# Kernel tuning notes

Measured on AMD Instinct MI355X. Metric: run time of the kernel, lower is better.

## Reference

```python
import jax, jax.numpy as jnp
import numpy as np

NUM_HEADS = 16
HEAD_DIM = 80  # head_dim_ori; NPU pads 80->128 with zeros (math-neutral)


def _rotate_half(x):
    x1, x2 = jnp.split(x, 2, axis=-1)
    return jnp.concatenate([-x2, x1], axis=-1)


def setup_inputs() -> dict:
    key = jax.random.key(0)
    ks = jax.random.split(key, 7)
    S, E = 4096, 1280
    inv = jnp.asarray(1.0 / np.sqrt(E), jnp.float32)
    # rotary tables: proper cos/sin from angles for realism
    pos = jnp.arange(S, dtype=jnp.float32)[:, None]
    freqs = 1.0 / (10000.0 ** (jnp.arange(0, HEAD_DIM // 2, dtype=jnp.float32) / (HEAD_DIM // 2)))
    ang = pos * freqs[None, :]                      # [S, 40]
    ang = jnp.concatenate([ang, ang], axis=-1)      # [S, 80] rotate-half layout
    return {
        'hidden_states': jax.random.normal(ks[0], (S, E), jnp.float32),
        'cos': jnp.cos(ang),
        'sin': jnp.sin(ang),
        'w_qkv': jax.random.normal(ks[1], (3 * E, E), jnp.float32) * inv,
        'b_qkv': jax.random.normal(ks[2], (3 * E,), jnp.float32) * 0.02,
        'w_proj': jax.random.normal(ks[3], (E, E), jnp.float32) * inv,
        'b_proj': jax.random.normal(ks[4], (E,), jnp.float32) * 0.02,
    }


def reference(hidden_states, cos, sin, w_qkv, b_qkv, w_proj, b_proj):
    S, E = hidden_states.shape
    H, D = NUM_HEADS, HEAD_DIM
    # fused QKV linear (transposeB=True, hasBias=True) then split into 3
    qkv = hidden_states @ w_qkv.T + b_qkv          # [S, 3E]
    q, k, v = jnp.split(qkv, 3, axis=-1)
    q = q.reshape(S, H, D)
    k = k.reshape(S, H, D)
    v = v.reshape(S, H, D)
    # rotate-half RoPE (rotaryCoeff=2) on q and k
    c = cos[:, None, :]
    s = sin[:, None, :]
    q = q * c + _rotate_half(q) * s
    k = k * c + _rotate_half(k) * s
    # full bidirectional self-attention (PA_ENCODER), qkScale = 1/sqrt(head_dim_ori)
    scale = jnp.asarray(1.0 / np.sqrt(D), q.dtype)
    scores = jnp.einsum('shd,thd->hst', q, k) * scale   # [H, S, S]
    attn = jax.nn.softmax(scores, axis=-1)
    out = jnp.einsum('hst,thd->shd', attn, v).reshape(S, E)
    # output projection + residual add (atten_res_add)
    dense = out @ w_proj.T + b_proj
    return hidden_states + dense
```

## Files before the change

### kernel.cpp

```cpp
#include <hip/hip_runtime.h>
#include <hip/hip_bf16.h>


#define S_LEN 4096
#define E_DIM 1280
#define NH 16
#define HD 80
#define HDP 96

typedef __bf16 bf16x8 __attribute__((ext_vector_type(8)));
typedef float f32x4 __attribute__((ext_vector_type(4)));

__device__ __forceinline__ short f2bf(float x) {
    __hip_bfloat16 h = __float2bfloat16(x);
    return __builtin_bit_cast(short, h);
}
__device__ __forceinline__ float bf2f(short x) {
    return __bfloat162float(__builtin_bit_cast(__hip_bfloat16, x));
}
__device__ __forceinline__ bf16x8 ldb(const short* p) {
    return *reinterpret_cast<const bf16x8*>(p);
}
__device__ __forceinline__ unsigned cvt_pk_bf16(float a, float b) {
    unsigned r;
    asm("v_cvt_pk_bf16_f32 %0, %1, %2" : "=v"(r) : "v"(a), "v"(b));
    return r;
}
__device__ __forceinline__ void gload16(const void* g, void* l) {
    __builtin_amdgcn_global_load_lds(
        (const __attribute__((address_space(1))) unsigned int*)g,
        (__attribute__((address_space(3))) unsigned int*)l, 16, 0, 0);
}

__global__ __launch_bounds__(256) void cast3_k(const float* __restrict__ a, short* __restrict__ oa, int na4,
                                               const float* __restrict__ b, short* __restrict__ ob, int nb4,
                                               const float* __restrict__ c, short* __restrict__ oc, int nc4) {
    int j = blockIdx.x * 256 + threadIdx.x;
    const float* src;
    short* dst;
    if (j < na4) {
        src = a; dst = oa;
    } else {
        j -= na4;
        if (j < nb4) {
            src = b; dst = ob;
        } else {
            j -= nb4;
            if (j >= nc4) return;
            src = c; dst = oc;
        }
    }
    float4 v = *reinterpret_cast<const float4*>(&src[j * 4]);
    ushort4 o;
    o.x = (unsigned short)f2bf(v.x);
    o.y = (unsigned short)f2bf(v.y);
    o.z = (unsigned short)f2bf(v.z);
    o.w = (unsigned short)f2bf(v.w);
    *reinterpret_cast<ushort4*>(&dst[j * 4]) = o;
}

template <int MODE>
__global__ __launch_bounds__(256) void gemm_bt_k(
    const short* __restrict__ A, const short* __restrict__ B, const float* __restrict__ bias,
    short* __restrict__ Qraw, short* __restrict__ Kraw, short* __restrict__ Vg,
    const float* __restrict__ resid, float* __restrict__ Out) {
    const int K = E_DIM;
    __shared__ short As[2][128 * 64];
    __shared__ short Bs[2][128 * 64];
    int t = threadIdx.x;
    int lane = t & 63, w = t >> 6;
    int wr = w >> 1, wc = w & 1;
    int lr = lane & 15, lg = lane >> 4;
    int mb = blockIdx.y * 128, nb = blockIdx.x * 128;

    const short* asrc[4];
    const short* bsrc[4];
#pragma unroll
    for (int c = 0; c < 4; c++) {
        int p = c * 256 + t;
        int m = p >> 3;
        int kg = (p & 7) ^ (m & 7);
        asrc[c] = A + (size_t)(mb + m) * K + kg * 8;
        bsrc[c] = B + (size_t)(nb + m) * K + kg * 8;
    }
    int xa = lr & 7;
    int cx0 = ((0 * 4 + lg) ^ xa) * 8;
    int cx1 = ((1 * 4 + lg) ^ xa) * 8;
    int rowA[4], rowB[4];
#pragma unroll
    for (int i = 0; i < 4; i++) {
        rowA[i] = (wr * 64 + i * 16 + lr) * 64;
        rowB[i] = (wc * 64 + i * 16 + lr) * 64;
    }

    f32x4 acc[4][4];
#pragma unroll
    for (int i = 0; i < 4; i++)
#pragma unroll
        for (int j = 0; j < 4; j++) acc[i][j] = (f32x4){0.f, 0.f, 0.f, 0.f};

#define G_STAGE(buf, kb)                                             \
    {                                                                \
        _Pragma("unroll") for (int c = 0; c < 4; c++) {              \
            int ldso = c * 2048 + w * 512;                           \
            gload16(asrc[c] + (kb), &As[buf][ldso]);                 \
            gload16(bsrc[c] + (kb), &Bs[buf][ldso]);                 \
        }                                                            \
    }

    G_STAGE(0, 0);
    asm volatile("s_waitcnt vmcnt(0)" ::: "memory");
    __syncthreads();

    int buf = 0;
    for (int kb = 0; kb < K; kb += 64) {
        if (kb + 64 < K) G_STAGE(buf ^ 1, kb + 64);
        __builtin_amdgcn_s_setprio(1);
#pragma unroll
        for (int kk = 0; kk < 2; kk++) {
            int cx = kk ? cx1 : cx0;
            bf16x8 af[4], bfr[4];
#pragma unroll
            for (int i = 0; i < 4; i++) {
                af[i] = ldb(&As[buf][rowA[i] + cx]);
                bfr[i] = ldb(&Bs[buf][rowB[i] + cx]);
            }
#pragma unroll
            for (int i = 0; i < 4; i++)
#pragma unroll
                for (int j = 0; j < 4; j++)
                    acc[i][j] = __builtin_amdgcn_mfma_f32_16x16x32_bf16(af[i], bfr[j], acc[i][j], 0, 0, 0);
        }
        __builtin_amdgcn_s_setprio(0);
        __syncthreads();
        buf ^= 1;
    }
#undef G_STAGE

    if (MODE == 0) {
        int part = nb / E_DIM;
        short* dst = (part == 0) ? Qraw : (part == 1) ? Kraw : Vg;
#pragma unroll
        for (int j = 0; j < 4; j++) {
            int n = nb + wc * 64 + j * 16 + lr;
            float bv = bias[n];
            int hd = n - part * E_DIM;
            int h = hd / HD, d = hd - h * HD;
#pragma unroll
            for (int i = 0; i < 4; i++) {
#pragma unroll
                for (int r = 0; r < 4; r++) {
                    int s = mb + wr * 64 + i * 16 + lg * 4 + r;
                    dst[(h * S_LEN + s) * HD + d] = f2bf(acc[i][j][r] + bv);
                }
            }
        }
    } else {
#pragma unroll
        for (int j = 0; j < 4; j++) {
            int n = nb + wc * 64 + j * 16 + lr;
            float bv = bias[n];
#pragma unroll
            for (int i = 0; i < 4; i++) {
#pragma unroll
                for (int r = 0; r < 4; r++) {
                    int s = mb + wr * 64 + i * 16 + lg * 4 + r;
                    Out[s * E_DIM + n] = acc[i][j][r] + bv + resid[s * E_DIM + n];
                }
            }
        }
    }
}

__global__ __launch_bounds__(256) void rope_k(const short* __restrict__ Qraw,
                                              const short* __restrict__ Kraw,
                                              const float* __restrict__ cosp,
                                              const float* __restrict__ sinp,
                                              short* __restrict__ Qg, short* __restrict__ Kg) {
    int idx = blockIdx.x * 256 + threadIdx.x;
    int c = idx % 12;
    int sh = idx / 12;
    int s = sh & (S_LEN - 1);
    int base96 = sh * HDP + c * 8;
    if (c >= 10) {
        int4 z = {0, 0, 0, 0};
        *reinterpret_cast<int4*>(&Qg[base96]) = z;
        *reinterpret_cast<int4*>(&Kg[base96]) = z;
        return;
    }
    int d0 = c * 8;
    int dp = (d0 < 40) ? d0 + 40 : d0 - 40;
    float sgn = (d0 < 40) ? -1.f : 1.f;
    int base80 = sh * HD;
    float q[8], qp[8], k[8], kp[8], cs[8], sn[8];
    {
        int4 v;
        v = *reinterpret_cast<const int4*>(&Qraw[base80 + d0]);
        const short* sp = reinterpret_cast<const short*>(&v);
        for (int i = 0; i < 8; i++) q[i] = bf2f(sp[i]);
        v = *reinterpret_cast<const int4*>(&Qraw[base80 + dp]);
        for (int i = 0; i < 8; i++) qp[i] = bf2f(sp[i]);
        v = *reinterpret_cast<const int4*>(&Kraw[base80 + d0]);
        for (int i = 0; i < 8; i++) k[i] = bf2f(sp[i]);
        v = *reinterpret_cast<const int4*>(&Kraw[base80 + dp]);
        for (int i = 0; i < 8; i++) kp[i] = bf2f(sp[i]);
    }
    *reinterpret_cast<float4*>(&cs[0]) = *reinterpret_cast<const float4*>(&cosp[s * HD + d0]);
    *reinterpret_cast<float4*>(&cs[4]) = *reinterpret_cast<const float4*>(&cosp[s * HD + d0 + 4]);
    *reinterpret_cast<float4*>(&sn[0]) = *reinterpret_cast<const float4*>(&sinp[s * HD + d0]);
    *reinterpret_cast<float4*>(&sn[4]) = *reinterpret_cast<const float4*>(&sinp[s * HD + d0 + 4]);
    const float qscale = 0.16129849190f;
    short oq[8], ok[8];
#pragma unroll
    for (int i = 0; i < 8; i++) {
        oq[i] = f2bf((q[i] * cs[i] + sgn * qp[i] * sn[i]) * qscale);
        ok[i] = f2bf(k[i] * cs[i] + sgn * kp[i] * sn[i]);
    }
    *reinterpret_cast<int4*>(&Qg[base96]) = *reinterpret_cast<int4*>(oq);
    *reinterpret_cast<int4*>(&Kg[base96]) = *reinterpret_cast<int4*>(ok);
}

__global__ __launch_bounds__(256) void transpose_v_k(const short* __restrict__ Vg,
                                                     short* __restrict__ Vt) {
    __shared__ short tile[32][33];
    int h = blockIdx.z, sb = blockIdx.x * 32, db = blockIdx.y * 32;
    int t = threadIdx.x;
    for (int e = t; e < 1024; e += 256) {
        int si = e >> 5, dj = e & 31;
        int d = db + dj;
        tile[si][dj] = (d < HD) ? Vg[(h * S_LEN + sb + si) * HD + d] : (short)0;
    }
    __syncthreads();
    for (int e = t; e < 1024; e += 256) {
        int di = e >> 5, sj = e & 31;
        int d = db + di;
        if (d < HD) Vt[(h * HD + d) * S_LEN + sb + sj] = tile[sj][di];
    }
}

__global__ __launch_bounds__(512, 4) void attn_k(const short* __restrict__ Qg,
                                                 const short* __restrict__ Kg,
                                                 const short* __restrict__ Vt,
                                                 short* __restrict__ Ob) {
    __shared__ __align__(16) short smem[35072];
    short* ksb = smem;
    short* vsb = smem + 13312;
    short* psb = smem + 24832;

    int t = threadIdx.x;
    int lane = t & 63, w = t >> 6;
    int lr = lane & 15, lg = lane >> 4;
    int pairi = w >> 1, half = w & 1;
    int L = blockIdx.x;
    int h = ((L & 7) << 1) | (L >> 8);
    int qb = ((L >> 3) & 31) << 7;

    const short* kgp = Kg + (size_t)h * S_LEN * HDP;
    const short* vgp = Vt + (size_t)h * HD * S_LEN;

    bf16x8 qf[2][3];
#pragma unroll
    for (int qq = 0; qq < 2; qq++) {
        const short* qp = Qg + ((size_t)h * S_LEN + qb + pairi * 32 + qq * 16 + lr) * HDP;
#pragma unroll
        for (int kk = 0; kk < 3; kk++) qf[qq][kk] = ldb(qp + kk * 32 + lg * 8);
    }
    f32x4 o[2][5];
#pragma unroll
    for (int qq = 0; qq < 2; qq++)
#pragma unroll
        for (int nd = 0; nd < 5; nd++) o[qq][nd] = (f32x4){0.f, 0.f, 0.f, 0.f};
    f32x4 l4[2] = {(f32x4){0.f, 0.f, 0.f, 0.f}, (f32x4){0.f, 0.f, 0.f, 0.f}};

    int gk0 = t, rk0 = gk0 / 13, ok0 = gk0 % 13;
    if (ok0 == 12) ok0 = 0;
    const short* ksrc0 = kgp + rk0 * HDP + ok0 * 8;
    int gk1 = t + 512, rk1 = gk1 / 13, ok1 = gk1 % 13;
    if (ok1 == 12) ok1 = 0;
    const short* ksrc1 = kgp + rk1 * HDP + ok1 * 8;
    int gv0 = t, rv0 = gv0 / 9, ov0 = gv0 % 9;
    if (ov0 == 8) ov0 = 0;
    const short* vsrc0 = vgp + (size_t)rv0 * S_LEN + ov0 * 8;
    bool v1v = (t + 512) < 720;
    int gv1 = t + 512, rv1 = gv1 / 9, ov1 = gv1 % 9;
    if (ov1 == 8) ov1 = 0;
    const short* vsrc1 = vgp + (size_t)rv1 * S_LEN + ov1 * 8;

#define A_STAGE(buf, kb)                                                          \
    {                                                                             \
        gload16(ksrc0 + (size_t)(kb) * HDP, ksb + (buf)*6656 + w * 512);          \
        if (w < 5) gload16(ksrc1 + (size_t)(kb) * HDP, ksb + (buf)*6656 + 4096 + w * 512); \
        gload16(vsrc0 + (kb), vsb + (buf)*5760 + w * 512);                        \
        if (v1v) gload16(vsrc1 + (kb), vsb + (buf)*5760 + 4096 + w * 512);        \
    }

    A_STAGE(0, 0);
    asm volatile("s_waitcnt vmcnt(0)" ::: "memory");
    __syncthreads();

    short* ps = psb + w * 1280;
    int buf = 0;
    for (int kb = 0; kb < S_LEN; kb += 64) {
        if (kb + 64 < S_LEN) A_STAGE(buf ^ 1, kb + 64);
        const short* ks = ksb + buf * 6656;
        const short* vs = vsb + buf * 5760;

        f32x4 sc[2][2];
#pragma unroll
        for (int qq = 0; qq < 2; qq++)
#pragma unroll
            for (int n = 0; n < 2; n++) sc[qq][n] = (f32x4){0.f, 0.f, 0.f, 0.f};
        __builtin_amdgcn_s_setprio(1);
#pragma unroll
        for (int n = 0; n < 2; n++) {
#pragma unroll
            for (int kk = 0; kk < 3; kk++) {
                bf16x8 kf = ldb(&ks[(half * 32 + n * 16 + lr) * 104 + kk * 32 + lg * 8]);
                sc[0][n] = __builtin_amdgcn_mfma_f32_16x16x32_bf16(kf, qf[0][kk], sc[0][n], 0, 0, 0);
                sc[1][n] = __builtin_amdgcn_mfma_f32_16x16x32_bf16(kf, qf[1][kk], sc[1][n], 0, 0, 0);
            }
        }
        __builtin_amdgcn_s_setprio(0);

#pragma unroll
        for (int qq = 0; qq < 2; qq++) {
#pragma unroll
            for (int n = 0; n < 2; n++) {
#pragma unroll
                for (int r = 0; r < 4; r++) sc[qq][n][r] = __builtin_amdgcn_exp2f(sc[qq][n][r]);
                l4[qq] += sc[qq][n];
                uint2 pk;
                pk.x = cvt_pk_bf16(sc[qq][n][0], sc[qq][n][1]);
                pk.y = cvt_pk_bf16(sc[qq][n][2], sc[qq][n][3]);
                *reinterpret_cast<uint2*>(&ps[(qq * 16 + lr) * 40 + n * 16 + lg * 4]) = pk;
            }
        }

        bf16x8 pf0 = ldb(&ps[(0 * 16 + lr) * 40 + lg * 8]);
        bf16x8 pf1 = ldb(&ps[(1 * 16 + lr) * 40 + lg * 8]);
        __builtin_amdgcn_s_setprio(1);
#pragma unroll
        for (int nd = 0; nd < 5; nd++) {
            bf16x8 vf = ldb(&vs[(nd * 16 + lr) * 72 + half * 32 + lg * 8]);
            o[0][nd] = __builtin_amdgcn_mfma_f32_16x16x32_bf16(pf0, vf, o[0][nd], 0, 0, 0);
            o[1][nd] = __builtin_amdgcn_mfma_f32_16x16x32_bf16(pf1, vf, o[1][nd], 0, 0, 0);
        }
        __builtin_amdgcn_s_setprio(0);

        __syncthreads();
        buf ^= 1;
    }
#undef A_STAGE

    float lh[2];
#pragma unroll
    for (int qq = 0; qq < 2; qq++) {
        float l = l4[qq][0] + l4[qq][1] + l4[qq][2] + l4[qq][3];
        l += __shfl_xor(l, 16);
        l += __shfl_xor(l, 32);
        lh[qq] = l;
    }
    float* Osc = reinterpret_cast<float*>(smem);
    float* lsc = reinterpret_cast<float*>(smem) + 10240;
    if (half) {
#pragma unroll
        for (int qq = 0; qq < 2; qq++) {
#pragma unroll
            for (int nd = 0; nd < 5; nd++)
#pragma unroll
                for (int r = 0; r < 4; r++)
                    Osc[(pairi * 32 + qq * 16 + lg * 4 + r) * 80 + nd * 16 + lr] = o[qq][nd][r];
            if (lg == 0) lsc[pairi * 32 + qq * 16 + lr] = lh[qq];
        }
    }
    __syncthreads();
    if (!half) {
        float rl[2][4];
#pragma unroll
        for (int qq = 0; qq < 2; qq++) {
            float lt = lh[qq] + lsc[pairi * 32 + qq * 16 + lr];
#pragma unroll
            for (int r = 0; r < 4; r++) {
                float lf = __shfl(lt, lg * 4 + r);
                rl[qq][r] = __builtin_amdgcn_rcpf(lf);
            }
        }
#pragma unroll
        for (int qq = 0; qq < 2; qq++)
#pragma unroll
            for (int nd = 0; nd < 5; nd++)
#pragma unroll
                for (int r = 0; r < 4; r++) {
                    int s = qb + pairi * 32 + qq * 16 + lg * 4 + r;
                    float val = o[qq][nd][r] + Osc[(pairi * 32 + qq * 16 + lg * 4 + r) * 80 + nd * 16 + lr];
                    Ob[s * E_DIM + h * HD + nd * 16 + lr] = f2bf(val * rl[qq][r]);
                }
    }
}

extern "C" void kernel_launch(void* const* d_in, const int* in_sizes, int n_in,
                              void* d_out, int out_size, void* d_ws, size_t ws_size,
                              hipStream_t stream) {
    const float* hidden = (const float*)d_in[0];
    const float* cosp = (const float*)d_in[1];
    const float* sinp = (const float*)d_in[2];
    const float* wqkv = (const float*)d_in[3];
    const float* bqkv = (const float*)d_in[4];
    const float* wproj = (const float*)d_in[5];
    const float* bproj = (const float*)d_in[6];
    float* out = (float*)d_out;

    char* p = (char*)d_ws;
    short* Xb = (short*)p;      p += (size_t)S_LEN * E_DIM * 2;
    short* Wqkvb = (short*)p;   p += (size_t)3 * E_DIM * E_DIM * 2;
    short* Wprojb = (short*)p;  p += (size_t)E_DIM * E_DIM * 2;
    short* Qraw = (short*)p;    p += (size_t)NH * S_LEN * HD * 2;
    short* Kraw = (short*)p;    p += (size_t)NH * S_LEN * HD * 2;
    short* Vg = (short*)p;      p += (size_t)NH * S_LEN * HD * 2;
    short* Qg = (short*)p;      p += (size_t)NH * S_LEN * HDP * 2;
    short* Kg = (short*)p;      p += (size_t)NH * S_LEN * HDP * 2;
    short* Vt = (short*)p;      p += (size_t)NH * HD * S_LEN * 2;
    short* Ob = Xb;

    const int na4 = S_LEN * E_DIM / 4;
    const int nb4 = 3 * E_DIM * E_DIM / 4;
    const int nc4 = E_DIM * E_DIM / 4;
    cast3_k<<<(na4 + nb4 + nc4 + 255) / 256, 256, 0, stream>>>(
        hidden, Xb, na4, wqkv, Wqkvb, nb4, wproj, Wprojb, nc4);

    gemm_bt_k<0><<<dim3(3 * E_DIM / 128, S_LEN / 128), 256, 0, stream>>>(
        Xb, Wqkvb, bqkv, Qraw, Kraw, Vg, nullptr, nullptr);

    rope_k<<<NH * S_LEN * 12 / 256, 256, 0, stream>>>(Qraw, Kraw, cosp, sinp, Qg, Kg);

    transpose_v_k<<<dim3(S_LEN / 32, 3, NH), 256, 0, stream>>>(Vg, Vt);

    attn_k<<<dim3(512), 512, 0, stream>>>(Qg, Kg, Vt, Ob);

    gemm_bt_k<1><<<dim3(E_DIM / 128, S_LEN / 128), 256, 0, stream>>>(
        Ob, Wprojb, bproj, nullptr, nullptr, nullptr, hidden, out);
}
```

Before: 212.2 us.

## Add dedicated 256x256-tile QKV GEMM kernel with 8 waves and block swizzle

Replaces the templated 128x128 QKV projection GEMM with a new kernel that uses 256x256 output tiles, 512 threads (8 waves) and a hand-scheduled double-buffered LDS pipeline split into K-halves with explicit waitcnt/barriers. Blocks are remapped with a swizzle, and the grid of 240 blocks roughly matches the CU count. The larger tiles cut global and LDS traffic per FLOP, and the interleaved staging is meant to hide load latency. In exchange it uses more registers and LDS per block, and the handwritten synchronisation is fragile. The output-projection GEMM is de-templated but otherwise unchanged.

```diff
diff --git a/kernel.cpp b/kernel.cpp
--- a/kernel.cpp
+++ b/kernel.cpp
@@ -59,10 +59,171 @@
     *reinterpret_cast<ushort4*>(&dst[j * 4]) = o;
 }
 
-template <int MODE>
+__global__ __launch_bounds__(512, 2) void gemm1_256_k(
+    const short* __restrict__ A, const short* __restrict__ B, const float* __restrict__ bias,
+    short* __restrict__ Qraw, short* __restrict__ Kraw, short* __restrict__ Vg) {
+    const int K = E_DIM;
+    __shared__ short As[2][2][8192];
+    __shared__ short Bs[2][2][8192];
+    int t = threadIdx.x;
+    int lane = t & 63, w = t >> 6;
+    int wr = w >> 2, wc = w & 3;
+    int lr = lane & 15, lg = lane >> 4;
+    int bid = blockIdx.x;
+    int swz = (bid & 7) * 30 + (bid >> 3);
+    int bm = swz / 15, bn = swz % 15;
+    int mb = bm * 256, nb = bn * 256;
+
+    int lgs = (t & 3) ^ ((t >> 3) & 3);
+    const short* aS = A + (size_t)(mb + (t >> 2)) * K + lgs * 8;
+    const short* bS = B + (size_t)(nb + (t >> 2)) * K + lgs * 8;
+    const int rowStep = 128 * K;
+
+    int aoff[2][4], boff[4];
+#pragma unroll
+    for (int mq = 0; mq < 2; mq++)
+#pragma unroll
+        for (int ii = 0; ii < 4; ii++) {
+            int r = wr * 128 + mq * 64 + ii * 16 + lr;
+            aoff[mq][ii] = r * 32 + ((lg ^ ((r >> 1) & 3)) * 8);
+        }
+#pragma unroll
+    for (int n = 0; n < 4; n++) {
+        int r = wc * 64 + n * 16 + lr;
+        boff[n] = r * 32 + ((lg ^ ((r >> 1) & 3)) * 8);
+    }
+
+    f32x4 acc[8][4];
+#pragma unroll
+    for (int i = 0; i < 8; i++)
+#pragma unroll
+        for (int n = 0; n < 4; n++) acc[i][n] = (f32x4){0.f, 0.f, 0.f, 0.f};
+
+#define STG_A(d, kh, kb2)                                              \
+    {                                                                  \
+        gload16(aS + (kb2) + (kh)*32, &As[d][kh][w * 512]);            \
+        gload16(aS + rowStep + (kb2) + (kh)*32, &As[d][kh][4096 + w * 512]); \
+    }
+#define STG_B(d, kh, kb2)                                              \
+    {                                                                  \
+        gload16(bS + (kb2) + (kh)*32, &Bs[d][kh][w * 512]);            \
+        gload16(bS + rowStep + (kb2) + (kh)*32, &Bs[d][kh][4096 + w * 512]); \
+    }
+
+    STG_A(0, 0, 0);
+    STG_B(0, 0, 0);
+    STG_A(0, 1, 0);
+    STG_B(0, 1, 0);
+    asm volatile("s_waitcnt vmcnt(4)" ::: "memory");
+    __builtin_amdgcn_s_barrier();
+    asm volatile("" ::: "memory");
+
+    for (int kb = 0; kb < K; kb += 64) {
+        int d = (kb >> 6) & 1;
+        int kb2 = kb + 64;
+        bool more = kb2 < K;
+        bf16x8 af[4], bfr[4];
+
+#pragma unroll
+        for (int n = 0; n < 4; n++) bfr[n] = ldb(&Bs[d][0][boff[n]]);
+#pragma unroll
+        for (int ii = 0; ii < 4; ii++) af[ii] = ldb(&As[d][0][aoff[0][ii]]);
+        if (more) STG_A(d ^ 1, 0, kb2);
+        __builtin_amdgcn_s_barrier();
+        asm volatile("s_waitcnt lgkmcnt(0)" ::: "memory");
+        __builtin_amdgcn_sched_barrier(0);
+        __builtin_amdgcn_s_setprio(1);
+#pragma unroll
+        for (int ii = 0; ii < 4; ii++)
+#pragma unroll
+            for (int n = 0; n < 4; n++)
+                acc[ii][n] = __builtin_amdgcn_mfma_f32_16x16x32_bf16(af[ii], bfr[n], acc[ii][n], 0, 0, 0);
+        __builtin_amdgcn_s_setprio(0);
+        __builtin_amdgcn_s_barrier();
+        asm volatile("" ::: "memory");
+
+#pragma unroll
+        for (int ii = 0; ii < 4; ii++) af[ii] = ldb(&As[d][0][aoff[1][ii]]);
+        if (more) {
+            STG_B(d ^ 1, 0, kb2);
+            asm volatile("s_waitcnt vmcnt(4)" ::: "memory");
+        } else {
+            asm volatile("s_waitcnt vmcnt(0)" ::: "memory");
+        }
+        __builtin_amdgcn_s_barrier();
+        asm volatile("s_waitcnt lgkmcnt(0)" ::: "memory");
+        __builtin_amdgcn_sched_barrier(0);
+        __builtin_amdgcn_s_setprio(1);
+#pragma unroll
+        for (int ii = 0; ii < 4; ii++)
+#pragma unroll
+            for (int n = 0; n < 4; n++)
+                acc[4 + ii][n] = __builtin_amdgcn_mfma_f32_16x16x32_bf16(af[ii], bfr[n], acc[4 + ii][n], 0, 0, 0);
+        __builtin_amdgcn_s_setprio(0);
+        __builtin_amdgcn_s_barrier();
+        asm volatile("" ::: "memory");
+
+#pragma unroll
+        for (int n = 0; n < 4; n++) bfr[n] = ldb(&Bs[d][1][boff[n]]);
+#pragma unroll
+        for (int ii = 0; ii < 4; ii++) af[ii] = ldb(&As[d][1][aoff[0][ii]]);
+        if (more) STG_A(d ^ 1, 1, kb2);
+        __builtin_amdgcn_s_barrier();
+        asm volatile("s_waitcnt lgkmcnt(0)" ::: "memory");
+        __builtin_amdgcn_sched_barrier(0);
+        __builtin_amdgcn_s_setprio(1);
+#pragma unroll
+        for (int ii = 0; ii < 4; ii++)
+#pragma unroll
+            for (int n = 0; n < 4; n++)
+                acc[ii][n] = __builtin_amdgcn_mfma_f32_16x16x32_bf16(af[ii], bfr[n], acc[ii][n], 0, 0, 0);
+        __builtin_amdgcn_s_setprio(0);
+        __builtin_amdgcn_s_barrier();
+        asm volatile("" ::: "memory");
+
+#pragma unroll
+        for (int ii = 0; ii < 4; ii++) af[ii] = ldb(&As[d][1][aoff[1][ii]]);
+        if (more) {
+            STG_B(d ^ 1, 1, kb2);
+            asm volatile("s_waitcnt vmcnt(4)" ::: "memory");
+        }
+        __builtin_amdgcn_s_barrier();
+        asm volatile("s_waitcnt lgkmcnt(0)" ::: "memory");
+        __builtin_amdgcn_sched_barrier(0);
+        __builtin_amdgcn_s_setprio(1);
+#pragma unroll
+        for (int ii = 0; ii < 4; ii++)
+#pragma unroll
+            for (int n = 0; n < 4; n++)
+                acc[4 + ii][n] = __builtin_amdgcn_mfma_f32_16x16x32_bf16(af[ii], bfr[n], acc[4 + ii][n], 0, 0, 0);
+        __builtin_amdgcn_s_setprio(0);
+        __builtin_amdgcn_s_barrier();
+        asm volatile("" ::: "memory");
+    }
+#undef STG_A
+#undef STG_B
+
+    int part = nb / E_DIM;
+    short* dst = (part == 0) ? Qraw : (part == 1) ? Kraw : Vg;
+#pragma unroll
+    for (int j = 0; j < 4; j++) {
+        int n = nb + wc * 64 + j * 16 + lr;
+        float bv = bias[n];
+        int hd = n - part * E_DIM;
+        int h = hd / HD, dd = hd - h * HD;
+#pragma unroll
+        for (int i = 0; i < 8; i++) {
+#pragma unroll
+            for (int r = 0; r < 4; r++) {
+                int s = mb + wr * 128 + (i >> 2) * 64 + (i & 3) * 16 + lg * 4 + r;
+                dst[(h * S_LEN + s) * HD + dd] = f2bf(acc[i][j][r] + bv);
+            }
+        }
+    }
+}
+
 __global__ __launch_bounds__(256) void gemm_bt_k(
     const short* __restrict__ A, const short* __restrict__ B, const float* __restrict__ bias,
-    short* __restrict__ Qraw, short* __restrict__ Kraw, short* __restrict__ Vg,
     const float* __restrict__ resid, float* __restrict__ Out) {
     const int K = E_DIM;
     __shared__ short As[2][128 * 64];
@@ -137,36 +298,16 @@
     }
 #undef G_STAGE
 
-    if (MODE == 0) {
-        int part = nb / E_DIM;
-        short* dst = (part == 0) ? Qraw : (part == 1) ? Kraw : Vg;
-#pragma unroll
-        for (int j = 0; j < 4; j++) {
-            int n = nb + wc * 64 + j * 16 + lr;
-            float bv = bias[n];
-            int hd = n - part * E_DIM;
-            int h = hd / HD, d = hd - h * HD;
-#pragma unroll
-            for (int i = 0; i < 4; i++) {
-#pragma unroll
-                for (int r = 0; r < 4; r++) {
-                    int s = mb + wr * 64 + i * 16 + lg * 4 + r;
-                    dst[(h * S_LEN + s) * HD + d] = f2bf(acc[i][j][r] + bv);
-                }
-            }
-        }
-    } else {
-#pragma unroll
-        for (int j = 0; j < 4; j++) {
-            int n = nb + wc * 64 + j * 16 + lr;
-            float bv = bias[n];
-#pragma unroll
-            for (int i = 0; i < 4; i++) {
-#pragma unroll
-                for (int r = 0; r < 4; r++) {
-                    int s = mb + wr * 64 + i * 16 + lg * 4 + r;
-                    Out[s * E_DIM + n] = acc[i][j][r] + bv + resid[s * E_DIM + n];
-                }
+#pragma unroll
+    for (int j = 0; j < 4; j++) {
+        int n = nb + wc * 64 + j * 16 + lr;
+        float bv = bias[n];
+#pragma unroll
+        for (int i = 0; i < 4; i++) {
+#pragma unroll
+            for (int r = 0; r < 4; r++) {
+                int s = mb + wr * 64 + i * 16 + lg * 4 + r;
+                Out[s * E_DIM + n] = acc[i][j][r] + bv + resid[s * E_DIM + n];
             }
         }
     }
@@ -428,8 +569,7 @@
     cast3_k<<<(na4 + nb4 + nc4 + 255) / 256, 256, 0, stream>>>(
         hidden, Xb, na4, wqkv, Wqkvb, nb4, wproj, Wprojb, nc4);
 
-    gemm_bt_k<0><<<dim3(3 * E_DIM / 128, S_LEN / 128), 256, 0, stream>>>(
-        Xb, Wqkvb, bqkv, Qraw, Kraw, Vg, nullptr, nullptr);
+    gemm1_256_k<<<dim3(240), 512, 0, stream>>>(Xb, Wqkvb, bqkv, Qraw, Kraw, Vg);
 
     rope_k<<<NH * S_LEN * 12 / 256, 256, 0, stream>>>(Qraw, Kraw, cosp, sinp, Qg, Kg);
 
@@ -437,6 +577,6 @@
 
     attn_k<<<dim3(512), 512, 0, stream>>>(Qg, Kg, Vt, Ob);
 
-    gemm_bt_k<1><<<dim3(E_DIM / 128, S_LEN / 128), 256, 0, stream>>>(
-        Ob, Wprojb, bproj, nullptr, nullptr, nullptr, hidden, out);
-}
+    gemm_bt_k<<<dim3(E_DIM / 128, S_LEN / 128), 256, 0, stream>>>(
+        Ob, Wprojb, bproj, hidden, out);
+}
```

New measurement: 206.5 us. -2.7%, faster.
